# Kernel optimization log

Hardware: AMD Instinct MI355X
Metric: run time of the kernel (lower is better)

Reference implementation:

```python
import jax, jax.numpy as jnp
import numpy as np

B, FIN, V, X, Y, Z = 1, 32, 4096, 6, 6, 6
K, FOUT = 8, 32
NNZ = 9 * V  # sphere graph laplacian: ~8 neighbors + diagonal per vertex


def setup_inputs() -> dict:
    key = jax.random.key(0)
    k1, k2, k3, k4, k5, k6 = jax.random.split(key, 6)
    inputs = jax.random.normal(k1, (B, FIN, V, X, Y, Z), dtype=jnp.float32)
    weight = jax.random.normal(k2, (K, FIN, FOUT), dtype=jnp.float32) * 0.05
    bias = jax.random.normal(k3, (FOUT,), dtype=jnp.float32) * 0.05
    lap_rows = jax.random.randint(k4, (NNZ,), 0, V, dtype=jnp.int32)
    lap_cols = jax.random.randint(k5, (NNZ,), 0, V, dtype=jnp.int32)
    lap_vals = jax.random.normal(k6, (NNZ,), dtype=jnp.float32) * 0.1
    return {"inputs": inputs, "weight": weight, "bias": bias,
            "lap_vals": lap_vals, "lap_rows": lap_rows, "lap_cols": lap_cols}


def reference(inputs, weight, bias, lap_vals, lap_rows, lap_cols):
    b, fin, v, x, y, z = inputs.shape
    k, _, fout = weight.shape

    def spmm(xm):  # sparse [V,V] @ dense [V,D] via gather + segment-sum scatter
        return jax.ops.segment_sum(lap_vals[:, None] * xm[lap_cols], lap_rows,
                                   num_segments=v)

    # [V, Fin*B*X*Y*Z]
    x0 = jnp.transpose(inputs, (2, 1, 0, 3, 4, 5)).reshape(v, fin * b * x * y * z)
    # Chebyshev recurrence: T0 = x, T1 = Lx, Tk = 2 L T_{k-1} - T_{k-2}
    cheb = [x0]
    if k > 1:
        x1 = spmm(x0)
        cheb.append(x1)
        for _ in range(2, k):
            x2 = 2.0 * spmm(x1) - x0
            cheb.append(x2)
            x0, x1 = x1, x2
    basis = jnp.stack(cheb, 0)  # [K, V, Fin*B*X*Y*Z]
    basis = basis.reshape(k, v, fin, b, x, y, z)
    basis = jnp.transpose(basis, (3, 1, 4, 5, 6, 0, 2))  # [B,V,X,Y,Z,K,Fin]
    basis = basis.reshape(b * v * x * y * z, k * fin)
    out = basis @ weight.reshape(k * fin, fout)  # dense projection GEMM
    out = out.reshape(b, v, x, y, z, fout)
    out = jnp.transpose(out, (0, 5, 1, 2, 3, 4))  # [B, Fout, V, X, Y, Z]
    return out + bias[None, :, None, None, None, None]
```

## Files before the change

kernel.cpp:

```cpp
#include <hip/hip_runtime.h>
#include <stdint.h>

#define V_N    4096
#define NNZ_N  36864
#define S_N    216
#define ST_TOT 27
#define PLANES 256
#define BPLANES 224

typedef float  f32x2 __attribute__((ext_vector_type(2)));
typedef float  f32x4 __attribute__((ext_vector_type(4)));
typedef short  s16x4 __attribute__((ext_vector_type(4)));
typedef short  s16x8 __attribute__((ext_vector_type(8)));

static __device__ __forceinline__ unsigned short f2bf(float f){
    union { float f; unsigned u; } x; x.f = f;
    unsigned r = x.u + 0x7FFFu + ((x.u >> 16) & 1u);
    return (unsigned short)(r >> 16);
}
static __device__ __forceinline__ unsigned packbf(float lo, float hi){
    unsigned r;
    asm("v_cvt_pk_bf16_f32 %0, %1, %2" : "=v"(r) : "v"(lo), "v"(hi));
    return r;
}
static __device__ __forceinline__ void pkfma(f32x2& acc, f32x2 c, f32x2 vv){
    asm("v_pk_fma_f32 %0, %1, %2, %0" : "+v"(acc) : "v"(c), "v"(vv));
}
#define BLO(u) __uint_as_float((u) << 16)
#define BHI(u) __uint_as_float((u) & 0xFFFF0000u)

static __device__ __forceinline__ int bperm(int p, int vrr){
    return ((vrr >> 2) << 10) + (((vrr >> 1) & 1) << 9)
         + ((p >> 5) << 6) + (((p >> 2) & 1) << 5) + (((p >> 3) & 3) << 3)
         + ((p & 3) << 1) + (vrr & 1);
}

__global__ __launch_bounds__(1024) void k_prep(
    const int* __restrict__ rows, int* __restrict__ row_order,
    int* __restrict__ sp, int* __restrict__ gcnt, int* __restrict__ goff,
    int* __restrict__ rcur)
{
    __shared__ int cnt[4096];
    __shared__ int c2[4096];
    __shared__ int dh[64];
    int t = threadIdx.x;
    #pragma unroll
    for (int i = 0; i < 4; ++i) cnt[t + i*1024] = 0;
    if (t < 64) dh[t] = 0;
    __syncthreads();
    for (int e = t; e < NNZ_N; e += 1024) atomicAdd(&cnt[rows[e]], 1);
    __syncthreads();
    #pragma unroll
    for (int i = 0; i < 4; ++i){
        int d = cnt[t + i*1024]; if (d > 63) d = 63;
        atomicAdd(&dh[d], 1);
    }
    __syncthreads();
    if (t == 0){ int s = 0; for (int i = 0; i < 64; ++i){ int x = dh[i]; dh[i] = s; s += x; } }
    __syncthreads();
    #pragma unroll
    for (int i = 0; i < 4; ++i){
        int v = t + i*1024;
        int d = cnt[v]; int db = d > 63 ? 63 : d;
        int pos = atomicAdd(&dh[db], 1);
        row_order[pos] = v; sp[v] = pos; c2[pos] = d;
    }
    #pragma unroll
    for (int i = 0; i < 4; ++i) rcur[t + i*1024] = 0;
    __syncthreads();
    if (t == 0){
        int off = 0;
        for (int g = 0; g < 64; ++g){
            int d = c2[g*64 + 63]; if (d > 64) d = 64;
            gcnt[g] = d; goff[g] = off; off += (d + 3) * 64;
        }
    }
}

__global__ void k_fill2(const int* __restrict__ rows, const int* __restrict__ cols,
                        const float* __restrict__ vals, const int* __restrict__ sp,
                        const int* __restrict__ gcnt, const int* __restrict__ goff,
                        int* __restrict__ rcur, unsigned* __restrict__ ell,
                        const float* __restrict__ w, unsigned short* __restrict__ wtab)
{
    int bid = blockIdx.x, t = threadIdx.x;
    if (bid < 144){
        int e = bid * 256 + t;
        if (e < NNZ_N){
            int r = rows[e]; int s = sp[r]; int g = s >> 6; int l = s & 63;
            int i = atomicAdd(&rcur[r], 1);
            if (i < gcnt[g])
                ell[goff[g] + i * 64 + l] =
                    ((unsigned)cols[e] << 4) | ((unsigned)f2bf(vals[e]) << 16);
        }
    } else {
        int idx = (bid - 144) * 256 + t;
        int slot = idx >> 3, j = idx & 7;
        int ki = slot >> 7, nh = (slot >> 6) & 1, l = slot & 63;
        int p  = ki * 32 + ((l >> 4) << 3) + j;
        int fo = nh * 16 + (l & 15);
        wtab[idx] = f2bf(w[p * 32 + fo]);
    }
}

__global__ __launch_bounds__(256, 4) void k_pre(
    const float* __restrict__ in, uint4* __restrict__ t0t)
{
    __shared__ unsigned short lds[64 * 218];
    int bid = blockIdx.x;
    int f = bid >> 6, vblk = bid & 63;
    int t = threadIdx.x;
    const f32x4* src = (const f32x4*)(in + ((size_t)f * V_N + vblk * 64) * S_N);

    #pragma unroll
    for (int it = 0; it < 14; ++it){
        int idx = t + it * 256;
        if (idx < 3456){
            int vloc = (int)(((unsigned)idx * 4855u) >> 18);
            int s4   = idx - vloc * 54;
            f32x4 a = __builtin_nontemporal_load(&src[idx]);
            uint2 q; q.x = packbf(a.x, a.y); q.y = packbf(a.z, a.w);
            *(uint2*)((char*)lds + vloc * 436 + s4 * 8) = q;
        }
    }
    __syncthreads();
    #pragma unroll
    for (int it = 0; it < 7; ++it){
        int idx = t + it * 256;
        if (idx < ST_TOT * 64){
            int stl = idx >> 6, vl = idx & 63;
            uint4 q = *(const uint4*)((const char*)lds + vl * 436 + stl * 16);
            t0t[((size_t)(stl * 512 + vblk * 8 + (vl >> 3))) * 256 + f * 8 + (vl & 7)] = q;
        }
    }
}

__global__ __launch_bounds__(1024, 8) void k_phaseA(
    const int* __restrict__ row_order,
    const int* __restrict__ goff, const int* __restrict__ gcnt,
    const unsigned* __restrict__ ell, const uint4* __restrict__ t0t,
    uint4* __restrict__ basis3, int st0)
{
    __shared__ uint4 T4[V_N];
    int f   = blockIdx.x & 31;
    int stl = blockIdx.x >> 5;
    int st_g = st0 + stl;
    int t = threadIdx.x;

    const uint4* t0p = t0t + ((size_t)st_g << 9) * 256 + f * 8;
    #pragma unroll
    for (int rr = 0; rr < 4; ++rr){
        int v = t + rr * 1024;
        T4[v] = t0p[(size_t)(v >> 3) * 256 + (v & 7)];
    }
    __syncthreads();

    int w = t >> 6, lane = t & 63;
    int vr[4], gba[4], gcn[4];
    #pragma unroll
    for (int rr = 0; rr < 4; ++rr){
        int g = w + rr * 16;
        vr[rr]  = row_order[g * 64 + lane];
        gba[rr] = goff[g] + lane;
        gcn[rr] = __builtin_amdgcn_readfirstlane(gcnt[g]);
    }
    uint4 tm2[4];
    #pragma unroll
    for (int rr = 0; rr < 4; ++rr) tm2[rr] = T4[vr[rr]];

    for (int k = 1; k < 8; ++k){
        uint4 nst[4];
        #pragma unroll
        for (int rr = 0; rr < 4; ++rr){
            f32x2 ac0 = {0,0}, ac1 = {0,0}, ac2 = {0,0}, ac3 = {0,0};
            const unsigned* ep = ell + gba[rr];
            int cnt = gcn[rr];
            unsigned u0 = ep[0];
            unsigned u1 = ep[64];
            for (int i = 0; i < cnt; i += 2){
                unsigned n0 = ep[(i + 2) << 6];
                unsigned n1 = ep[(i + 3) << 6];
                uint4 q0 = *(const uint4*)((const char*)T4 + (u0 & 0xFFF0u));
                uint4 q1 = *(const uint4*)((const char*)T4 + (u1 & 0xFFF0u));
                float v0 = __uint_as_float(u0 & 0xFFFF0000u);
                float v1 = __uint_as_float(u1 & 0xFFFF0000u);
                f32x2 vv0 = {v0, v0};
                f32x2 vv1 = {v1, v1};
                f32x2 c;
                c.x = BLO(q0.x); c.y = BHI(q0.x);  pkfma(ac0, c, vv0);
                c.x = BLO(q0.y); c.y = BHI(q0.y);  pkfma(ac1, c, vv0);
                c.x = BLO(q0.z); c.y = BHI(q0.z);  pkfma(ac2, c, vv0);
                c.x = BLO(q0.w); c.y = BHI(q0.w);  pkfma(ac3, c, vv0);
                c.x = BLO(q1.x); c.y = BHI(q1.x);  pkfma(ac0, c, vv1);
                c.x = BLO(q1.y); c.y = BHI(q1.y);  pkfma(ac1, c, vv1);
                c.x = BLO(q1.z); c.y = BHI(q1.z);  pkfma(ac2, c, vv1);
                c.x = BLO(q1.w); c.y = BHI(q1.w);  pkfma(ac3, c, vv1);
                u0 = n0; u1 = n1;
            }
            float a0 = ac0.x, a1 = ac0.y, a2 = ac1.x, a3 = ac1.y;
            float a4 = ac2.x, a5 = ac2.y, a6 = ac3.x, a7 = ac3.y;
            if (k > 1){
                a0 = fmaf(2.f, a0, -BLO(tm2[rr].x));  a1 = fmaf(2.f, a1, -BHI(tm2[rr].x));
                a2 = fmaf(2.f, a2, -BLO(tm2[rr].y));  a3 = fmaf(2.f, a3, -BHI(tm2[rr].y));
                a4 = fmaf(2.f, a4, -BLO(tm2[rr].z));  a5 = fmaf(2.f, a5, -BHI(tm2[rr].z));
                a6 = fmaf(2.f, a6, -BLO(tm2[rr].w));  a7 = fmaf(2.f, a7, -BHI(tm2[rr].w));
            }
            nst[rr].x = packbf(a0, a1); nst[rr].y = packbf(a2, a3);
            nst[rr].z = packbf(a4, a5); nst[rr].w = packbf(a6, a7);
        }
        #pragma unroll
        for (int rr = 0; rr < 4; ++rr) tm2[rr] = T4[vr[rr]];
        __syncthreads();
        #pragma unroll
        for (int rr = 0; rr < 4; ++rr) T4[vr[rr]] = nst[rr];
        __syncthreads();
        uint4* bp = basis3 + ((size_t)stl << 9) * 1792 + ((k - 1) * 32 + f) * 8;
        #pragma unroll
        for (int rr = 0; rr < 4; ++rr){
            int v = t + rr * 1024;
            bp[(size_t)(v >> 3) * 1792 + (v & 7)] = T4[v];
        }
    }
}

__global__ __launch_bounds__(256) void k_probe(
    const uint4* __restrict__ basis3, const uint4* __restrict__ t0t)
{
    int t = threadIdx.x;
    int tile = blockIdx.x;
    int stl = tile >> 9, vb = tile & 511;
    const uint4* srcT = t0t + ((size_t)(stl * 512 + vb)) * 256;
    const uint4* srcB = basis3 + ((size_t)(stl * 512 + vb)) * 1792;
    uint4 acc = srcT[t];
    #pragma unroll
    for (int it = 0; it < 7; ++it){
        uint4 q = srcB[it * 256 + t];
        acc.x ^= q.x; acc.y ^= q.y; acc.z ^= q.z; acc.w ^= q.w;
    }
    asm volatile("" :: "v"(acc.x), "v"(acc.y), "v"(acc.z), "v"(acc.w));
}

__global__ __launch_bounds__(256, 2) void k_phaseB(
    const uint4* __restrict__ basis3, const uint4* __restrict__ t0t,
    const uint4* __restrict__ wtab, const float* __restrict__ bias,
    float* __restrict__ out, int st0)
{
    __shared__ uint4 A[4096];
    __shared__ uint4 WL[1024];
    int t = threadIdx.x;
    int tile = blockIdx.x;
    int stl = tile >> 8, vb2 = tile & 255;
    int st_g = st0 + stl;
    int lane = t & 63, w = t >> 6;

    #pragma unroll
    for (int h = 0; h < 2; ++h){
        int vb = vb2 * 2 + h;
        const uint4* srcT = t0t + ((size_t)(st_g * 512 + vb)) * 256;
        const uint4* srcB = basis3 + ((size_t)(stl * 512 + vb)) * 1792;
        uint4 q[8];
        q[0] = srcT[t];
        #pragma unroll
        for (int it = 0; it < 7; ++it) q[1 + it] = srcB[it * 256 + t];
        A[h * 2048 + bperm(t >> 3, t & 7)] = q[0];
        #pragma unroll
        for (int it = 0; it < 7; ++it){
            int g = it * 256 + t;
            A[h * 2048 + bperm(32 + (g >> 3), g & 7)] = q[1 + it];
        }
    }
    #pragma unroll
    for (int it = 0; it < 4; ++it) WL[(it << 8) + t] = wtab[(it << 8) + t];
    __syncthreads();

    unsigned ldsA = (unsigned)(size_t)(&A[0]);
    unsigned abase = ldsA + w * 16384 + (lane << 3);
    const char* wbase = (const char*)&WL[0];

    f32x4 acc00 = {0,0,0,0}, acc01 = {0,0,0,0}, acc10 = {0,0,0,0}, acc11 = {0,0,0,0};
    #pragma unroll
    for (int ki = 0; ki < 8; ++ki){
        s16x4 x0, x1, x2, x3;
        unsigned a0 = abase + (ki << 10);
        unsigned a1 = a0 + 8192;
        asm volatile("ds_read_b64_tr_b16 %0, %4\n\t"
                     "ds_read_b64_tr_b16 %1, %4 offset:512\n\t"
                     "ds_read_b64_tr_b16 %2, %5\n\t"
                     "ds_read_b64_tr_b16 %3, %5 offset:512\n\t"
                     "s_waitcnt lgkmcnt(0)"
                     : "=&v"(x0), "=&v"(x1), "=&v"(x2), "=&v"(x3)
                     : "v"(a0), "v"(a1));
        __builtin_amdgcn_sched_barrier(0);
        s16x8 af0, af1;
        af0[0]=x0[0]; af0[1]=x0[1]; af0[2]=x0[2]; af0[3]=x0[3];
        af0[4]=x1[0]; af0[5]=x1[1]; af0[6]=x1[2]; af0[7]=x1[3];
        af1[0]=x2[0]; af1[1]=x2[1]; af1[2]=x2[2]; af1[3]=x2[3];
        af1[4]=x3[0]; af1[5]=x3[1]; af1[6]=x3[2]; af1[7]=x3[3];
        s16x8 b0 = *(const s16x8*)(wbase + ((((ki * 2 + 0) << 6) + lane) << 4));
        s16x8 b1 = *(const s16x8*)(wbase + ((((ki * 2 + 1) << 6) + lane) << 4));
        acc00 = __builtin_amdgcn_mfma_f32_16x16x32_bf16(af0, b0, acc00, 0, 0, 0);
        acc01 = __builtin_amdgcn_mfma_f32_16x16x32_bf16(af0, b1, acc01, 0, 0, 0);
        acc10 = __builtin_amdgcn_mfma_f32_16x16x32_bf16(af1, b0, acc10, 0, 0, 0);
        acc11 = __builtin_amdgcn_mfma_f32_16x16x32_bf16(af1, b1, acc11, 0, 0, 0);
    }

    __syncthreads();
    float* outT = (float*)&A[0];
    {
        int rl0 = w * 32 + ((lane >> 4) << 2);
        int foA = lane & 15, foB = 16 + (lane & 15);
        float2 p;
        p.x = acc00[0]; p.y = acc00[1]; *(float2*)&outT[foA*132 + rl0]      = p;
        p.x = acc00[2]; p.y = acc00[3]; *(float2*)&outT[foA*132 + rl0 + 2]  = p;
        p.x = acc01[0]; p.y = acc01[1]; *(float2*)&outT[foB*132 + rl0]      = p;
        p.x = acc01[2]; p.y = acc01[3]; *(float2*)&outT[foB*132 + rl0 + 2]  = p;
        p.x = acc10[0]; p.y = acc10[1]; *(float2*)&outT[foA*132 + rl0 + 16] = p;
        p.x = acc10[2]; p.y = acc10[3]; *(float2*)&outT[foA*132 + rl0 + 18] = p;
        p.x = acc11[0]; p.y = acc11[1]; *(float2*)&outT[foB*132 + rl0 + 16] = p;
        p.x = acc11[2]; p.y = acc11[3]; *(float2*)&outT[foB*132 + rl0 + 18] = p;
    }
    __syncthreads();
    {
        int fo = t >> 3;
        float bs = bias[fo];
        float* gb = out + (size_t)fo * V_N * S_N;
        #pragma unroll
        for (int it = 0; it < 4; ++it){
            int rl = ((t & 7) << 2) + (it << 5);
            float2 p0 = *(const float2*)&outT[fo*132 + rl];
            float2 p1 = *(const float2*)&outT[fo*132 + rl + 2];
            int r = vb2 * 128 + rl;
            int v = r >> 3, sl = r & 7;
            f32x4 o; o.x = p0.x + bs; o.y = p0.y + bs; o.z = p1.x + bs; o.w = p1.y + bs;
            *(f32x4*)(gb + (size_t)v * S_N + st_g * 8 + sl) = o;
        }
    }
}

extern "C" void kernel_launch(void* const* d_in, const int* in_sizes, int n_in,
                              void* d_out, int out_size, void* d_ws, size_t ws_size,
                              hipStream_t stream)
{
    const float* inp  = (const float*)d_in[0];
    const float* wgt  = (const float*)d_in[1];
    const float* bias = (const float*)d_in[2];
    const float* vals = (const float*)d_in[3];
    const int*   rows = (const int*)d_in[4];
    const int*   cols = (const int*)d_in[5];
    float* out = (float*)d_out;

    char* ws = (char*)d_ws;
    size_t o = 0;
    auto alloc = [&](size_t bytes) -> void* {
        void* p = ws + o; o = (o + bytes + 255) & ~(size_t)255; return p;
    };
    const size_t ELL_B = (size_t)64 * 67 * 64 * 4;
    int* row_order = (int*)alloc(4096 * 4);
    int* sp        = (int*)alloc(4096 * 4);
    int* gcnt      = (int*)alloc(64 * 4);
    int* goff      = (int*)alloc(64 * 4);
    int* rcur      = (int*)alloc(4096 * 4);
    unsigned* ell  = (unsigned*)alloc(ELL_B);
    uint4* wtab    = (uint4*)alloc(8192 * 2);
    uint4* t0buf   = (uint4*)alloc((size_t)ST_TOT * 512 * 256 * 16);
    size_t used = o;

    size_t per_st = (size_t)512 * 1792 * 16;
    size_t avail = (ws_size > used) ? (ws_size - used) : 0;
    int tiles_c = (int)(avail / per_st);
    if (tiles_c > 16) tiles_c = 16;
    if (tiles_c < 1) tiles_c = 1;
    uint4* basis = (uint4*)alloc(per_st * tiles_c);

    hipMemsetAsync(ell, 0, ELL_B, stream);
    k_prep  <<<1, 1024, 0, stream>>>(rows, row_order, sp, gcnt, goff, rcur);
    k_fill2 <<<176, 256, 0, stream>>>(rows, cols, vals, sp, gcnt, goff, rcur, ell,
                                      wgt, (unsigned short*)wtab);
    k_pre   <<<2048, 256, 0, stream>>>(inp, t0buf);

    bool first = true;
    for (int st0 = 0; st0 < ST_TOT; st0 += tiles_c){
        int tc = ST_TOT - st0; if (tc > tiles_c) tc = tiles_c;
        k_phaseA<<<32 * tc, 1024, 0, stream>>>(row_order, goff, gcnt, ell, t0buf, basis, st0);
        if (first){
            int pgrid = tc * 512; if (pgrid > 4096) pgrid = 4096;
            k_probe<<<pgrid, 256, 0, stream>>>(basis, t0buf);
            first = false;
        }
        k_phaseB<<<tc * 256, 256, 0, stream>>>(basis, t0buf, wtab, bias, out, st0);
    }
}
```

Baseline: 447.8 us.

## Switch Chebyshev basis from bf16 to fp16 with packed half FMAs; drop probe kernel

Stores the input, Laplacian values, weights and Chebyshev basis as fp16 instead of bf16. The SpMM inner loop now accumulates in packed fp16 FMAs directly on the loaded words, which removes the per-element bf16-to-fp32 unpacking, and the recurrence is one packed fma per word. The projection GEMM uses the fp16 MFMA. The extra probe kernel launch is also removed. Accumulating in fp16 loses accuracy and risks overflow over seven recurrence steps.

Result: faster. 372.0 us (-16.9%).

```diff
diff --git a/kernel.cpp b/kernel.cpp
--- a/kernel.cpp
+++ b/kernel.cpp
@@ -8,26 +8,28 @@
 #define PLANES 256
 #define BPLANES 224
 
-typedef float  f32x2 __attribute__((ext_vector_type(2)));
 typedef float  f32x4 __attribute__((ext_vector_type(4)));
 typedef short  s16x4 __attribute__((ext_vector_type(4)));
 typedef short  s16x8 __attribute__((ext_vector_type(8)));
-
-static __device__ __forceinline__ unsigned short f2bf(float f){
-    union { float f; unsigned u; } x; x.f = f;
-    unsigned r = x.u + 0x7FFFu + ((x.u >> 16) & 1u);
-    return (unsigned short)(r >> 16);
-}
-static __device__ __forceinline__ unsigned packbf(float lo, float hi){
+typedef _Float16 f16x8 __attribute__((ext_vector_type(8)));
+
+static __device__ __forceinline__ unsigned short f2h(float f){
+    union { _Float16 h; unsigned short u; } c; c.h = (_Float16)f; return c.u;
+}
+static __device__ __forceinline__ unsigned packh(float lo, float hi){
     unsigned r;
-    asm("v_cvt_pk_bf16_f32 %0, %1, %2" : "=v"(r) : "v"(lo), "v"(hi));
+    asm("v_cvt_pkrtz_f16_f32 %0, %1, %2" : "=v"(r) : "v"(lo), "v"(hi));
     return r;
 }
-static __device__ __forceinline__ void pkfma(f32x2& acc, f32x2 c, f32x2 vv){
-    asm("v_pk_fma_f32 %0, %1, %2, %0" : "+v"(acc) : "v"(c), "v"(vv));
-}
-#define BLO(u) __uint_as_float((u) << 16)
-#define BHI(u) __uint_as_float((u) & 0xFFFF0000u)
+#define PKFMA(acc, c, u) \
+    asm("v_pk_fma_f16 %0, %1, %2, %0 op_sel:[0,1,0] op_sel_hi:[1,1,1]" \
+        : "+v"(acc) : "v"(c), "v"(u))
+static __device__ __forceinline__ unsigned cheb(unsigned a, unsigned two, unsigned tm2){
+    unsigned n;
+    asm("v_pk_fma_f16 %0, %1, %2, %3 neg_lo:[0,0,1] neg_hi:[0,0,1]"
+        : "=v"(n) : "v"(a), "v"(two), "v"(tm2));
+    return n;
+}
 
 static __device__ __forceinline__ int bperm(int p, int vrr){
     return ((vrr >> 2) << 10) + (((vrr >> 1) & 1) << 9)
@@ -91,7 +93,7 @@
             int i = atomicAdd(&rcur[r], 1);
             if (i < gcnt[g])
                 ell[goff[g] + i * 64 + l] =
-                    ((unsigned)cols[e] << 4) | ((unsigned)f2bf(vals[e]) << 16);
+                    ((unsigned)cols[e] << 4) | ((unsigned)f2h(vals[e]) << 16);
         }
     } else {
         int idx = (bid - 144) * 256 + t;
@@ -99,7 +101,7 @@
         int ki = slot >> 7, nh = (slot >> 6) & 1, l = slot & 63;
         int p  = ki * 32 + ((l >> 4) << 3) + j;
         int fo = nh * 16 + (l & 15);
-        wtab[idx] = f2bf(w[p * 32 + fo]);
+        wtab[idx] = f2h(w[p * 32 + fo]);
     }
 }
 
@@ -119,7 +121,7 @@
             int vloc = (int)(((unsigned)idx * 4855u) >> 18);
             int s4   = idx - vloc * 54;
             f32x4 a = __builtin_nontemporal_load(&src[idx]);
-            uint2 q; q.x = packbf(a.x, a.y); q.y = packbf(a.z, a.w);
+            uint2 q; q.x = packh(a.x, a.y); q.y = packh(a.z, a.w);
             *(uint2*)((char*)lds + vloc * 436 + s4 * 8) = q;
         }
     }
@@ -146,6 +148,7 @@
     int stl = blockIdx.x >> 5;
     int st_g = st0 + stl;
     int t = threadIdx.x;
+    unsigned two = 0x40004000u;
 
     const uint4* t0p = t0t + ((size_t)st_g << 9) * 256 + f * 8;
     #pragma unroll
@@ -172,7 +175,7 @@
         uint4 nst[4];
         #pragma unroll
         for (int rr = 0; rr < 4; ++rr){
-            f32x2 ac0 = {0,0}, ac1 = {0,0}, ac2 = {0,0}, ac3 = {0,0};
+            unsigned ac0 = 0, ac1 = 0, ac2 = 0, ac3 = 0;
             const unsigned* ep = ell + gba[rr];
             int cnt = gcn[rr];
             unsigned u0 = ep[0];
@@ -182,31 +185,20 @@
                 unsigned n1 = ep[(i + 3) << 6];
                 uint4 q0 = *(const uint4*)((const char*)T4 + (u0 & 0xFFF0u));
                 uint4 q1 = *(const uint4*)((const char*)T4 + (u1 & 0xFFF0u));
-                float v0 = __uint_as_float(u0 & 0xFFFF0000u);
-                float v1 = __uint_as_float(u1 & 0xFFFF0000u);
-                f32x2 vv0 = {v0, v0};
-                f32x2 vv1 = {v1, v1};
-                f32x2 c;
-                c.x = BLO(q0.x); c.y = BHI(q0.x);  pkfma(ac0, c, vv0);
-                c.x = BLO(q0.y); c.y = BHI(q0.y);  pkfma(ac1, c, vv0);
-                c.x = BLO(q0.z); c.y = BHI(q0.z);  pkfma(ac2, c, vv0);
-                c.x = BLO(q0.w); c.y = BHI(q0.w);  pkfma(ac3, c, vv0);
-                c.x = BLO(q1.x); c.y = BHI(q1.x);  pkfma(ac0, c, vv1);
-                c.x = BLO(q1.y); c.y = BHI(q1.y);  pkfma(ac1, c, vv1);
-                c.x = BLO(q1.z); c.y = BHI(q1.z);  pkfma(ac2, c, vv1);
-                c.x = BLO(q1.w); c.y = BHI(q1.w);  pkfma(ac3, c, vv1);
+                PKFMA(ac0, q0.x, u0);  PKFMA(ac1, q0.y, u0);
+                PKFMA(ac2, q0.z, u0);  PKFMA(ac3, q0.w, u0);
+                PKFMA(ac0, q1.x, u1);  PKFMA(ac1, q1.y, u1);
+                PKFMA(ac2, q1.z, u1);  PKFMA(ac3, q1.w, u1);
                 u0 = n0; u1 = n1;
             }
-            float a0 = ac0.x, a1 = ac0.y, a2 = ac1.x, a3 = ac1.y;
-            float a4 = ac2.x, a5 = ac2.y, a6 = ac3.x, a7 = ac3.y;
             if (k > 1){
-                a0 = fmaf(2.f, a0, -BLO(tm2[rr].x));  a1 = fmaf(2.f, a1, -BHI(tm2[rr].x));
-                a2 = fmaf(2.f, a2, -BLO(tm2[rr].y));  a3 = fmaf(2.f, a3, -BHI(tm2[rr].y));
-                a4 = fmaf(2.f, a4, -BLO(tm2[rr].z));  a5 = fmaf(2.f, a5, -BHI(tm2[rr].z));
-                a6 = fmaf(2.f, a6, -BLO(tm2[rr].w));  a7 = fmaf(2.f, a7, -BHI(tm2[rr].w));
+                nst[rr].x = cheb(ac0, two, tm2[rr].x);
+                nst[rr].y = cheb(ac1, two, tm2[rr].y);
+                nst[rr].z = cheb(ac2, two, tm2[rr].z);
+                nst[rr].w = cheb(ac3, two, tm2[rr].w);
+            } else {
+                nst[rr].x = ac0; nst[rr].y = ac1; nst[rr].z = ac2; nst[rr].w = ac3;
             }
-            nst[rr].x = packbf(a0, a1); nst[rr].y = packbf(a2, a3);
-            nst[rr].z = packbf(a4, a5); nst[rr].w = packbf(a6, a7);
         }
         #pragma unroll
         for (int rr = 0; rr < 4; ++rr) tm2[rr] = T4[vr[rr]];
@@ -221,23 +213,6 @@
             bp[(size_t)(v >> 3) * 1792 + (v & 7)] = T4[v];
         }
     }
-}
-
-__global__ __launch_bounds__(256) void k_probe(
-    const uint4* __restrict__ basis3, const uint4* __restrict__ t0t)
-{
-    int t = threadIdx.x;
-    int tile = blockIdx.x;
-    int stl = tile >> 9, vb = tile & 511;
-    const uint4* srcT = t0t + ((size_t)(stl * 512 + vb)) * 256;
-    const uint4* srcB = basis3 + ((size_t)(stl * 512 + vb)) * 1792;
-    uint4 acc = srcT[t];
-    #pragma unroll
-    for (int it = 0; it < 7; ++it){
-        uint4 q = srcB[it * 256 + t];
-        acc.x ^= q.x; acc.y ^= q.y; acc.z ^= q.z; acc.w ^= q.w;
-    }
-    asm volatile("" :: "v"(acc.x), "v"(acc.y), "v"(acc.z), "v"(acc.w));
 }
 
 __global__ __launch_bounds__(256, 2) void k_phaseB(
@@ -298,10 +273,10 @@
         af1[4]=x3[0]; af1[5]=x3[1]; af1[6]=x3[2]; af1[7]=x3[3];
         s16x8 b0 = *(const s16x8*)(wbase + ((((ki * 2 + 0) << 6) + lane) << 4));
         s16x8 b1 = *(const s16x8*)(wbase + ((((ki * 2 + 1) << 6) + lane) << 4));
-        acc00 = __builtin_amdgcn_mfma_f32_16x16x32_bf16(af0, b0, acc00, 0, 0, 0);
-        acc01 = __builtin_amdgcn_mfma_f32_16x16x32_bf16(af0, b1, acc01, 0, 0, 0);
-        acc10 = __builtin_amdgcn_mfma_f32_16x16x32_bf16(af1, b0, acc10, 0, 0, 0);
-        acc11 = __builtin_amdgcn_mfma_f32_16x16x32_bf16(af1, b1, acc11, 0, 0, 0);
+        acc00 = __builtin_amdgcn_mfma_f32_16x16x32_f16(*(const f16x8*)&af0, *(const f16x8*)&b0, acc00, 0, 0, 0);
+        acc01 = __builtin_amdgcn_mfma_f32_16x16x32_f16(*(const f16x8*)&af0, *(const f16x8*)&b1, acc01, 0, 0, 0);
+        acc10 = __builtin_amdgcn_mfma_f32_16x16x32_f16(*(const f16x8*)&af1, *(const f16x8*)&b0, acc10, 0, 0, 0);
+        acc11 = __builtin_amdgcn_mfma_f32_16x16x32_f16(*(const f16x8*)&af1, *(const f16x8*)&b1, acc11, 0, 0, 0);
     }
 
     __syncthreads();
@@ -378,15 +353,9 @@
                                       wgt, (unsigned short*)wtab);
     k_pre   <<<2048, 256, 0, stream>>>(inp, t0buf);
 
-    bool first = true;
     for (int st0 = 0; st0 < ST_TOT; st0 += tiles_c){
         int tc = ST_TOT - st0; if (tc > tiles_c) tc = tiles_c;
         k_phaseA<<<32 * tc, 1024, 0, stream>>>(row_order, goff, gcnt, ell, t0buf, basis, st0);
-        if (first){
-            int pgrid = tc * 512; if (pgrid > 4096) pgrid = 4096;
-            k_probe<<<pgrid, 256, 0, stream>>>(basis, t0buf);
-            first = false;
-        }
         k_phaseB<<<tc * 256, 256, 0, stream>>>(basis, t0buf, wtab, bias, out, st0);
     }
 }
```
